# Kernel tuning notes

Hardware: AMD Instinct MI355X
Metric: run time of the kernel (lower is better)

## Reference

```python
import jax, jax.numpy as jnp
import numpy as np

B, N, K = 16, 4096, 32

def setup_inputs() -> dict:
    key = jax.random.key(0)
    k0, k1, k2, k3, k4, k5 = jax.random.split(key, 6)
    frames_rot = jax.random.normal(k0, (B, N, 3, 3), jnp.float32)
    frames_trans = jax.random.normal(k1, (B, N, 3), jnp.float32)
    pair_rot = jax.random.normal(k2, (B, N, K, 3, 3), jnp.float32)
    pair_trans = jax.random.normal(k3, (B, N, K, 3), jnp.float32)
    confidences = jax.random.uniform(k4, (B, N, K, 1), jnp.float32)
    topology = jax.random.randint(k5, (B, N, K), 0, N, jnp.int32)
    return {"frames_rot": frames_rot, "frames_trans": frames_trans,
            "pair_rot": pair_rot, "pair_trans": pair_trans,
            "confidences": confidences, "topology": topology}


def _proj_with_svd(m):
    """Kabsch projection of batched [..., 3, 3] matrices onto SO(3) (det=+1)."""
    u, s, vh = jnp.linalg.svd(m, full_matrices=False)
    V = jnp.swapaxes(vh, -1, -2)
    d = jnp.sign(jnp.linalg.det(jnp.matmul(V, jnp.swapaxes(u, -1, -2))))  # [...]
    d3 = jnp.concatenate([jnp.ones(d.shape + (2,), m.dtype), d[..., None]], axis=-1)  # diag(1,1,d)
    # rot = V @ diag(1,1,d) @ u^T
    return jnp.einsum('...ik,...k,...jk->...ij', V, d3, u)


def reference(frames_rot, frames_trans, pair_rot, pair_trans, confidences, topology):
    # gather neighbor frames T_j: [B,N,K,3,3] / [B,N,K,3]
    gather = jax.vmap(lambda f, t: f[t])
    Tj_rot = gather(frames_rot, topology)
    Tj_trans = gather(frames_trans, topology)

    # normalized confidences p_ij over neighbors K
    w = jnp.squeeze(confidences, axis=-1)             # [B,N,K]
    p = w / jnp.sum(w, axis=2, keepdims=True)         # [B,N,K]

    # compose rigids: T_j * T_ji
    comp_rot = jnp.einsum('bnkij,bnkjl->bnkil', Tj_rot, pair_rot)                 # [B,N,K,3,3]
    comp_trans = jnp.einsum('bnkij,bnkj->bnki', Tj_rot, pair_trans) + Tj_trans    # [B,N,K,3]

    # confidence-weighted average over neighbors
    avg_rot = jnp.einsum('bnk,bnkij->bnij', p, comp_rot)    # [B,N,3,3]
    avg_trans = jnp.einsum('bnk,bnki->bni', p, comp_trans)  # [B,N,3]

    # project averaged rot onto SO(3), then invert (transpose) as in the module
    rot = _proj_with_svd(avg_rot)
    rot_inv = jnp.swapaxes(rot, -1, -2)                     # invert_rots of a rotation

    # pack (rot 9 + trans 3) -> [B,N,12]
    return jnp.concatenate([rot_inv.reshape(B, N, 9), avg_trans], axis=-1)
```

## Files before the change

### kernel.cpp

```cpp
#include <hip/hip_runtime.h>
#include <math.h>

#define N_RES 4096
#define KNB 32
#define BN_TOTAL 65536

typedef float v4f __attribute__((ext_vector_type(4)));
typedef int v4i __attribute__((ext_vector_type(4)));

template <int p, int q>
__device__ __forceinline__ void jacobi_rot(float S[3][3], float V[3][3]) {
    float apq = S[p][q];
    if (fabsf(apq) > 1e-20f) {
        float app = S[p][p], aqq = S[q][q];
        float tau = (aqq - app) / (2.0f * apq);
        float tt = (tau >= 0.0f ? 1.0f : -1.0f) / (fabsf(tau) + sqrtf(1.0f + tau * tau));
        float c = 1.0f / sqrtf(1.0f + tt * tt);
        float s = tt * c;
#pragma unroll
        for (int i = 0; i < 3; i++) {
            float Sip = S[i][p], Siq = S[i][q];
            S[i][p] = c * Sip - s * Siq;
            S[i][q] = s * Sip + c * Siq;
        }
#pragma unroll
        for (int i = 0; i < 3; i++) {
            float Spi = S[p][i], Sqi = S[q][i];
            S[p][i] = c * Spi - s * Sqi;
            S[q][i] = s * Spi + c * Sqi;
        }
#pragma unroll
        for (int i = 0; i < 3; i++) {
            float Vip = V[i][p], Viq = V[i][q];
            V[i][p] = c * Vip - s * Viq;
            V[i][q] = s * Vip + c * Viq;
        }
    }
}

template <int A, int Bc>
__device__ __forceinline__ void sort_pair(float lam[3], float V[3][3]) {
    if (lam[A] < lam[Bc]) {
        float tl = lam[A]; lam[A] = lam[Bc]; lam[Bc] = tl;
#pragma unroll
        for (int i = 0; i < 3; i++) {
            float tv = V[i][A]; V[i][A] = V[i][Bc]; V[i][Bc] = tv;
        }
    }
}

__global__ __launch_bounds__(256) void backbone_kernel(
    const float* __restrict__ frames_rot,
    const float* __restrict__ frames_trans,
    const float* __restrict__ pair_rot,
    const float* __restrict__ pair_trans,
    const float* __restrict__ conf,
    const int* __restrict__ topo,
    float* __restrict__ out)
{
    int tid = threadIdx.x;
    int bid = blockIdx.x;

    int xcd = bid & 7;
    int slot = bid >> 3;
    int batch = xcd + ((slot >> 7) << 3);
    int chunk = slot & 127;

    int elem = batch * N_RES + chunk * 32 + (tid >> 3);
    int t = tid & 7;

    const float* fr_b = frames_rot + (size_t)batch * N_RES * 9;
    const float* ft_b = frames_trans + (size_t)batch * N_RES * 3;

    size_t kbase = (size_t)elem * KNB + (size_t)t * 4;
    const v4f* pr4 = (const v4f*)(pair_rot + kbase * 9);
    const v4f* pt4 = (const v4f*)(pair_trans + kbase * 3);
    const v4f* cf4 = (const v4f*)(conf + kbase);
    const v4i* tp4 = (const v4i*)(topo + kbase);

    float prl[36];
#pragma unroll
    for (int i = 0; i < 9; i++) {
        v4f v = __builtin_nontemporal_load(pr4 + i);
        prl[4 * i + 0] = v.x; prl[4 * i + 1] = v.y;
        prl[4 * i + 2] = v.z; prl[4 * i + 3] = v.w;
    }
    float ptl[12];
#pragma unroll
    for (int i = 0; i < 3; i++) {
        v4f v = __builtin_nontemporal_load(pt4 + i);
        ptl[4 * i + 0] = v.x; ptl[4 * i + 1] = v.y;
        ptl[4 * i + 2] = v.z; ptl[4 * i + 3] = v.w;
    }
    v4f wv = __builtin_nontemporal_load(cf4);
    float wl[4] = {wv.x, wv.y, wv.z, wv.w};
    v4i jv = __builtin_nontemporal_load(tp4);
    int jl[4] = {jv.x, jv.y, jv.z, jv.w};

    float Macc[9] = {0, 0, 0, 0, 0, 0, 0, 0, 0};
    float tacc[3] = {0, 0, 0};
    float wsum = 0.0f;

#pragma unroll
    for (int kk = 0; kk < 4; kk++) {
        int j = jl[kk];
        const float* Rj = fr_b + j * 9;
        const float* Tj = ft_b + j * 3;
        float r[9];
#pragma unroll
        for (int i = 0; i < 9; i++) r[i] = Rj[i];
        float tj[3];
#pragma unroll
        for (int i = 0; i < 3; i++) tj[i] = Tj[i];
        float w = wl[kk];
        const float* pr = prl + kk * 9;
        const float* pt = ptl + kk * 3;
#pragma unroll
        for (int i = 0; i < 3; i++) {
#pragma unroll
            for (int l = 0; l < 3; l++) {
                float cij = r[i * 3 + 0] * pr[0 * 3 + l] +
                            r[i * 3 + 1] * pr[1 * 3 + l] +
                            r[i * 3 + 2] * pr[2 * 3 + l];
                Macc[i * 3 + l] += w * cij;
            }
            float ct = r[i * 3 + 0] * pt[0] + r[i * 3 + 1] * pt[1] +
                       r[i * 3 + 2] * pt[2] + tj[i];
            tacc[i] += w * ct;
        }
        wsum += w;
    }

#pragma unroll
    for (int st = 1; st <= 4; st <<= 1) {
#pragma unroll
        for (int i = 0; i < 9; i++) Macc[i] += __shfl_xor(Macc[i], st);
#pragma unroll
        for (int i = 0; i < 3; i++) tacc[i] += __shfl_xor(tacc[i], st);
        wsum += __shfl_xor(wsum, st);
    }

    float inv_w = 1.0f / fmaxf(wsum, 1e-20f);
    float M[3][3];
#pragma unroll
    for (int i = 0; i < 3; i++)
#pragma unroll
        for (int j = 0; j < 3; j++) M[i][j] = Macc[i * 3 + j] * inv_w;
    float t0 = tacc[0] * inv_w, t1 = tacc[1] * inv_w, t2 = tacc[2] * inv_w;

    float S[3][3];
#pragma unroll
    for (int i = 0; i < 3; i++)
#pragma unroll
        for (int j = 0; j < 3; j++)
            S[i][j] = M[0][i] * M[0][j] + M[1][i] * M[1][j] + M[2][i] * M[2][j];
    float V[3][3] = {{1, 0, 0}, {0, 1, 0}, {0, 0, 1}};

#pragma unroll
    for (int sweep = 0; sweep < 4; sweep++) {
        jacobi_rot<0, 1>(S, V);
        jacobi_rot<0, 2>(S, V);
        jacobi_rot<1, 2>(S, V);
    }

    float lam[3] = {S[0][0], S[1][1], S[2][2]};
    sort_pair<0, 1>(lam, V);
    sort_pair<1, 2>(lam, V);
    sort_pair<0, 1>(lam, V);

    float detV = V[0][0] * (V[1][1] * V[2][2] - V[1][2] * V[2][1]) -
                 V[0][1] * (V[1][0] * V[2][2] - V[1][2] * V[2][0]) +
                 V[0][2] * (V[1][0] * V[2][1] - V[1][1] * V[2][0]);
    if (detV < 0.0f) { V[0][2] = -V[0][2]; V[1][2] = -V[1][2]; V[2][2] = -V[2][2]; }

    float Bm[3][3];
#pragma unroll
    for (int i = 0; i < 3; i++)
#pragma unroll
        for (int j = 0; j < 3; j++)
            Bm[i][j] = M[i][0] * V[0][j] + M[i][1] * V[1][j] + M[i][2] * V[2][j];

    float u0[3] = {Bm[0][0], Bm[1][0], Bm[2][0]};
    float n0 = u0[0] * u0[0] + u0[1] * u0[1] + u0[2] * u0[2];
    float rn0 = 1.0f / sqrtf(fmaxf(n0, 1e-24f));
    u0[0] *= rn0; u0[1] *= rn0; u0[2] *= rn0;

    float b1[3] = {Bm[0][1], Bm[1][1], Bm[2][1]};
    float d01 = u0[0] * b1[0] + u0[1] * b1[1] + u0[2] * b1[2];
    float u1[3] = {b1[0] - d01 * u0[0], b1[1] - d01 * u0[1], b1[2] - d01 * u0[2]};
    float n1 = u1[0] * u1[0] + u1[1] * u1[1] + u1[2] * u1[2];
    float rn1 = 1.0f / sqrtf(fmaxf(n1, 1e-24f));
    u1[0] *= rn1; u1[1] *= rn1; u1[2] *= rn1;

    float u2[3] = {u0[1] * u1[2] - u0[2] * u1[1],
                   u0[2] * u1[0] - u0[0] * u1[2],
                   u0[0] * u1[1] - u0[1] * u1[0]};

    float R[9];
#pragma unroll
    for (int i = 0; i < 3; i++) {
        float Ui0 = (i == 0 ? u0[0] : (i == 1 ? u0[1] : u0[2]));
        float Ui1 = (i == 0 ? u1[0] : (i == 1 ? u1[1] : u1[2]));
        float Ui2 = (i == 0 ? u2[0] : (i == 1 ? u2[1] : u2[2]));
#pragma unroll
        for (int j = 0; j < 3; j++)
            R[i * 3 + j] = Ui0 * V[j][0] + Ui1 * V[j][1] + Ui2 * V[j][2];
    }

    if (t == 0) {
        float4* o4 = (float4*)(out + (size_t)elem * 12);
        o4[0] = make_float4(R[0], R[1], R[2], R[3]);
        o4[1] = make_float4(R[4], R[5], R[6], R[7]);
        o4[2] = make_float4(R[8], t0, t1, t2);
    }
}

extern "C" void kernel_launch(void* const* d_in, const int* in_sizes, int n_in,
                              void* d_out, int out_size, void* d_ws, size_t ws_size,
                              hipStream_t stream) {
    const float* frames_rot = (const float*)d_in[0];
    const float* frames_trans = (const float*)d_in[1];
    const float* pair_rot = (const float*)d_in[2];
    const float* pair_trans = (const float*)d_in[3];
    const float* conf = (const float*)d_in[4];
    const int* topo = (const int*)d_in[5];
    float* out = (float*)d_out;

    dim3 grid(BN_TOTAL * 8 / 256), block(256);
    hipLaunchKernelGGL(backbone_kernel, grid, block, 0, stream,
                       frames_rot, frames_trans, pair_rot, pair_trans, conf, topo, out);
}
```

Before: 198.2 us.

## Split into repack, accumulate, and solve kernels with padded frame layout

Adds a repack kernel that copies frame rotation and translation into 16-float aligned rows so neighbour gathers become three 16-byte vector loads. Accumulation becomes its own kernel that writes per-element sums to workspace, and a separate solve kernel runs the Jacobi SVD projection with one thread per element, so seven of every eight lanes no longer sit idle through it. This costs two extra launches and extra workspace traffic for the repacked frames and accumulators. The original fused kernel is kept as a fallback when workspace is too small.

```diff
diff --git a/kernel.cpp b/kernel.cpp
--- a/kernel.cpp
+++ b/kernel.cpp
@@ -49,14 +49,96 @@
     }
 }
 
-__global__ __launch_bounds__(256) void backbone_kernel(
+__device__ __forceinline__ void project_and_store(const float M[3][3],
+                                                  float t0, float t1, float t2,
+                                                  float* outp) {
+    float S[3][3];
+#pragma unroll
+    for (int i = 0; i < 3; i++)
+#pragma unroll
+        for (int j = 0; j < 3; j++)
+            S[i][j] = M[0][i] * M[0][j] + M[1][i] * M[1][j] + M[2][i] * M[2][j];
+    float V[3][3] = {{1, 0, 0}, {0, 1, 0}, {0, 0, 1}};
+
+#pragma unroll
+    for (int sweep = 0; sweep < 4; sweep++) {
+        jacobi_rot<0, 1>(S, V);
+        jacobi_rot<0, 2>(S, V);
+        jacobi_rot<1, 2>(S, V);
+    }
+
+    float lam[3] = {S[0][0], S[1][1], S[2][2]};
+    sort_pair<0, 1>(lam, V);
+    sort_pair<1, 2>(lam, V);
+    sort_pair<0, 1>(lam, V);
+
+    float detV = V[0][0] * (V[1][1] * V[2][2] - V[1][2] * V[2][1]) -
+                 V[0][1] * (V[1][0] * V[2][2] - V[1][2] * V[2][0]) +
+                 V[0][2] * (V[1][0] * V[2][1] - V[1][1] * V[2][0]);
+    if (detV < 0.0f) { V[0][2] = -V[0][2]; V[1][2] = -V[1][2]; V[2][2] = -V[2][2]; }
+
+    float Bm[3][3];
+#pragma unroll
+    for (int i = 0; i < 3; i++)
+#pragma unroll
+        for (int j = 0; j < 3; j++)
+            Bm[i][j] = M[i][0] * V[0][j] + M[i][1] * V[1][j] + M[i][2] * V[2][j];
+
+    float u0[3] = {Bm[0][0], Bm[1][0], Bm[2][0]};
+    float n0 = u0[0] * u0[0] + u0[1] * u0[1] + u0[2] * u0[2];
+    float rn0 = 1.0f / sqrtf(fmaxf(n0, 1e-24f));
+    u0[0] *= rn0; u0[1] *= rn0; u0[2] *= rn0;
+
+    float b1[3] = {Bm[0][1], Bm[1][1], Bm[2][1]};
+    float d01 = u0[0] * b1[0] + u0[1] * b1[1] + u0[2] * b1[2];
+    float u1[3] = {b1[0] - d01 * u0[0], b1[1] - d01 * u0[1], b1[2] - d01 * u0[2]};
+    float n1 = u1[0] * u1[0] + u1[1] * u1[1] + u1[2] * u1[2];
+    float rn1 = 1.0f / sqrtf(fmaxf(n1, 1e-24f));
+    u1[0] *= rn1; u1[1] *= rn1; u1[2] *= rn1;
+
+    float u2[3] = {u0[1] * u1[2] - u0[2] * u1[1],
+                   u0[2] * u1[0] - u0[0] * u1[2],
+                   u0[0] * u1[1] - u0[1] * u1[0]};
+
+    float R[9];
+#pragma unroll
+    for (int i = 0; i < 3; i++) {
+        float Ui0 = (i == 0 ? u0[0] : (i == 1 ? u0[1] : u0[2]));
+        float Ui1 = (i == 0 ? u1[0] : (i == 1 ? u1[1] : u1[2]));
+        float Ui2 = (i == 0 ? u2[0] : (i == 1 ? u2[1] : u2[2]));
+#pragma unroll
+        for (int j = 0; j < 3; j++)
+            R[i * 3 + j] = Ui0 * V[j][0] + Ui1 * V[j][1] + Ui2 * V[j][2];
+    }
+
+    v4f* o4 = (v4f*)outp;
+    o4[0] = (v4f){R[0], R[1], R[2], R[3]};
+    o4[1] = (v4f){R[4], R[5], R[6], R[7]};
+    o4[2] = (v4f){R[8], t0, t1, t2};
+}
+
+__global__ __launch_bounds__(256) void repack_kernel(
     const float* __restrict__ frames_rot,
     const float* __restrict__ frames_trans,
+    float* __restrict__ pk)
+{
+    int row = blockIdx.x * 256 + threadIdx.x;
+    const float* fr = frames_rot + (size_t)row * 9;
+    const float* ft = frames_trans + (size_t)row * 3;
+    v4f a = {fr[0], fr[1], fr[2], fr[3]};
+    v4f b = {fr[4], fr[5], fr[6], fr[7]};
+    v4f c = {fr[8], ft[0], ft[1], ft[2]};
+    v4f* o = (v4f*)(pk + (size_t)row * 16);
+    o[0] = a; o[1] = b; o[2] = c;
+}
+
+__global__ __launch_bounds__(256) void accum_kernel(
+    const float* __restrict__ pk,
     const float* __restrict__ pair_rot,
     const float* __restrict__ pair_trans,
     const float* __restrict__ conf,
     const int* __restrict__ topo,
-    float* __restrict__ out)
+    float* __restrict__ acc)
 {
     int tid = threadIdx.x;
     int bid = blockIdx.x;
@@ -68,9 +150,6 @@
 
     int elem = batch * N_RES + chunk * 32 + (tid >> 3);
     int t = tid & 7;
-
-    const float* fr_b = frames_rot + (size_t)batch * N_RES * 9;
-    const float* ft_b = frames_trans + (size_t)batch * N_RES * 3;
 
     size_t kbase = (size_t)elem * KNB + (size_t)t * 4;
     const v4f* pr4 = (const v4f*)(pair_rot + kbase * 9);
@@ -101,17 +180,16 @@
     float tacc[3] = {0, 0, 0};
     float wsum = 0.0f;
 
+    size_t pkbase = (size_t)batch * N_RES * 16;
+
 #pragma unroll
     for (int kk = 0; kk < 4; kk++) {
         int j = jl[kk];
-        const float* Rj = fr_b + j * 9;
-        const float* Tj = ft_b + j * 3;
-        float r[9];
-#pragma unroll
-        for (int i = 0; i < 9; i++) r[i] = Rj[i];
-        float tj[3];
-#pragma unroll
-        for (int i = 0; i < 3; i++) tj[i] = Tj[i];
+        const v4f* row = (const v4f*)(pk + pkbase + (size_t)j * 16);
+        v4f fa = row[0], fb = row[1], fc = row[2];
+        float r[9] = {fa.x, fa.y, fa.z, fa.w, fb.x, fb.y, fb.z, fb.w, fc.x};
+        float tj[3] = {fc.y, fc.z, fc.w};
+
         float w = wl[kk];
         const float* pr = prl + kk * 9;
         const float* pt = ptl + kk * 3;
@@ -140,79 +218,121 @@
         wsum += __shfl_xor(wsum, st);
     }
 
+    if (t == 0) {
+        v4f* o = (v4f*)(acc + (size_t)elem * 16);
+        o[0] = (v4f){Macc[0], Macc[1], Macc[2], Macc[3]};
+        o[1] = (v4f){Macc[4], Macc[5], Macc[6], Macc[7]};
+        o[2] = (v4f){Macc[8], tacc[0], tacc[1], tacc[2]};
+        o[3] = (v4f){wsum, 0.0f, 0.0f, 0.0f};
+    }
+}
+
+__global__ __launch_bounds__(256) void solve_kernel(
+    const float* __restrict__ acc,
+    float* __restrict__ out)
+{
+    int elem = blockIdx.x * 256 + threadIdx.x;
+    const v4f* a4 = (const v4f*)(acc + (size_t)elem * 16);
+    v4f A0 = a4[0], A1 = a4[1], A2 = a4[2], A3 = a4[3];
+    float inv_w = 1.0f / fmaxf(A3.x, 1e-20f);
+    float M[3][3] = {{A0.x * inv_w, A0.y * inv_w, A0.z * inv_w},
+                     {A0.w * inv_w, A1.x * inv_w, A1.y * inv_w},
+                     {A1.z * inv_w, A1.w * inv_w, A2.x * inv_w}};
+    float t0 = A2.y * inv_w, t1 = A2.z * inv_w, t2 = A2.w * inv_w;
+    project_and_store(M, t0, t1, t2, out + (size_t)elem * 12);
+}
+
+__global__ __launch_bounds__(256) void fused_kernel(
+    const float* __restrict__ frames_rot, const float* __restrict__ frames_trans,
+    const float* __restrict__ pair_rot, const float* __restrict__ pair_trans,
+    const float* __restrict__ conf, const int* __restrict__ topo,
+    float* __restrict__ out)
+{
+    int tid = threadIdx.x;
+    int bid = blockIdx.x;
+    int xcd = bid & 7;
+    int slot = bid >> 3;
+    int batch = xcd + ((slot >> 7) << 3);
+    int chunk = slot & 127;
+    int elem = batch * N_RES + chunk * 32 + (tid >> 3);
+    int t = tid & 7;
+
+    const float* fr_b = frames_rot + (size_t)batch * N_RES * 9;
+    const float* ft_b = frames_trans + (size_t)batch * N_RES * 3;
+
+    size_t kbase = (size_t)elem * KNB + (size_t)t * 4;
+    const v4f* pr4 = (const v4f*)(pair_rot + kbase * 9);
+    const v4f* pt4 = (const v4f*)(pair_trans + kbase * 3);
+    const v4f* cf4 = (const v4f*)(conf + kbase);
+    const v4i* tp4 = (const v4i*)(topo + kbase);
+
+    float prl[36];
+#pragma unroll
+    for (int i = 0; i < 9; i++) {
+        v4f v = __builtin_nontemporal_load(pr4 + i);
+        prl[4 * i] = v.x; prl[4 * i + 1] = v.y; prl[4 * i + 2] = v.z; prl[4 * i + 3] = v.w;
+    }
+    float ptl[12];
+#pragma unroll
+    for (int i = 0; i < 3; i++) {
+        v4f v = __builtin_nontemporal_load(pt4 + i);
+        ptl[4 * i] = v.x; ptl[4 * i + 1] = v.y; ptl[4 * i + 2] = v.z; ptl[4 * i + 3] = v.w;
+    }
+    v4f wv = __builtin_nontemporal_load(cf4);
+    float wl[4] = {wv.x, wv.y, wv.z, wv.w};
+    v4i jv = __builtin_nontemporal_load(tp4);
+    int jl[4] = {jv.x, jv.y, jv.z, jv.w};
+
+    float Macc[9] = {0, 0, 0, 0, 0, 0, 0, 0, 0};
+    float tacc[3] = {0, 0, 0};
+    float wsum = 0.0f;
+
+#pragma unroll
+    for (int kk = 0; kk < 4; kk++) {
+        int j = jl[kk];
+        const float* Rj = fr_b + j * 9;
+        const float* Tj = ft_b + j * 3;
+        float r[9];
+#pragma unroll
+        for (int i = 0; i < 9; i++) r[i] = Rj[i];
+        float tj[3];
+#pragma unroll
+        for (int i = 0; i < 3; i++) tj[i] = Tj[i];
+        float w = wl[kk];
+        const float* pr = prl + kk * 9;
+        const float* pt = ptl + kk * 3;
+#pragma unroll
+        for (int i = 0; i < 3; i++) {
+#pragma unroll
+            for (int l = 0; l < 3; l++) {
+                float cij = r[i * 3] * pr[l] + r[i * 3 + 1] * pr[3 + l] + r[i * 3 + 2] * pr[6 + l];
+                Macc[i * 3 + l] += w * cij;
+            }
+            float ct = r[i * 3] * pt[0] + r[i * 3 + 1] * pt[1] + r[i * 3 + 2] * pt[2] + tj[i];
+            tacc[i] += w * ct;
+        }
+        wsum += w;
+    }
+
+#pragma unroll
+    for (int st = 1; st <= 4; st <<= 1) {
+#pragma unroll
+        for (int i = 0; i < 9; i++) Macc[i] += __shfl_xor(Macc[i], st);
+#pragma unroll
+        for (int i = 0; i < 3; i++) tacc[i] += __shfl_xor(tacc[i], st);
+        wsum += __shfl_xor(wsum, st);
+    }
+
     float inv_w = 1.0f / fmaxf(wsum, 1e-20f);
     float M[3][3];
 #pragma unroll
     for (int i = 0; i < 3; i++)
 #pragma unroll
         for (int j = 0; j < 3; j++) M[i][j] = Macc[i * 3 + j] * inv_w;
-    float t0 = tacc[0] * inv_w, t1 = tacc[1] * inv_w, t2 = tacc[2] * inv_w;
-
-    float S[3][3];
-#pragma unroll
-    for (int i = 0; i < 3; i++)
-#pragma unroll
-        for (int j = 0; j < 3; j++)
-            S[i][j] = M[0][i] * M[0][j] + M[1][i] * M[1][j] + M[2][i] * M[2][j];
-    float V[3][3] = {{1, 0, 0}, {0, 1, 0}, {0, 0, 1}};
-
-#pragma unroll
-    for (int sweep = 0; sweep < 4; sweep++) {
-        jacobi_rot<0, 1>(S, V);
-        jacobi_rot<0, 2>(S, V);
-        jacobi_rot<1, 2>(S, V);
-    }
-
-    float lam[3] = {S[0][0], S[1][1], S[2][2]};
-    sort_pair<0, 1>(lam, V);
-    sort_pair<1, 2>(lam, V);
-    sort_pair<0, 1>(lam, V);
-
-    float detV = V[0][0] * (V[1][1] * V[2][2] - V[1][2] * V[2][1]) -
-                 V[0][1] * (V[1][0] * V[2][2] - V[1][2] * V[2][0]) +
-                 V[0][2] * (V[1][0] * V[2][1] - V[1][1] * V[2][0]);
-    if (detV < 0.0f) { V[0][2] = -V[0][2]; V[1][2] = -V[1][2]; V[2][2] = -V[2][2]; }
-
-    float Bm[3][3];
-#pragma unroll
-    for (int i = 0; i < 3; i++)
-#pragma unroll
-        for (int j = 0; j < 3; j++)
-            Bm[i][j] = M[i][0] * V[0][j] + M[i][1] * V[1][j] + M[i][2] * V[2][j];
-
-    float u0[3] = {Bm[0][0], Bm[1][0], Bm[2][0]};
-    float n0 = u0[0] * u0[0] + u0[1] * u0[1] + u0[2] * u0[2];
-    float rn0 = 1.0f / sqrtf(fmaxf(n0, 1e-24f));
-    u0[0] *= rn0; u0[1] *= rn0; u0[2] *= rn0;
-
-    float b1[3] = {Bm[0][1], Bm[1][1], Bm[2][1]};
-    float d01 = u0[0] * b1[0] + u0[1] * b1[1] + u0[2] * b1[2];
-    float u1[3] = {b1[0] - d01 * u0[0], b1[1] - d01 * u0[1], b1[2] - d01 * u0[2]};
-    float n1 = u1[0] * u1[0] + u1[1] * u1[1] + u1[2] * u1[2];
-    float rn1 = 1.0f / sqrtf(fmaxf(n1, 1e-24f));
-    u1[0] *= rn1; u1[1] *= rn1; u1[2] *= rn1;
-
-    float u2[3] = {u0[1] * u1[2] - u0[2] * u1[1],
-                   u0[2] * u1[0] - u0[0] * u1[2],
-                   u0[0] * u1[1] - u0[1] * u1[0]};
-
-    float R[9];
-#pragma unroll
-    for (int i = 0; i < 3; i++) {
-        float Ui0 = (i == 0 ? u0[0] : (i == 1 ? u0[1] : u0[2]));
-        float Ui1 = (i == 0 ? u1[0] : (i == 1 ? u1[1] : u1[2]));
-        float Ui2 = (i == 0 ? u2[0] : (i == 1 ? u2[1] : u2[2]));
-#pragma unroll
-        for (int j = 0; j < 3; j++)
-            R[i * 3 + j] = Ui0 * V[j][0] + Ui1 * V[j][1] + Ui2 * V[j][2];
-    }
-
-    if (t == 0) {
-        float4* o4 = (float4*)(out + (size_t)elem * 12);
-        o4[0] = make_float4(R[0], R[1], R[2], R[3]);
-        o4[1] = make_float4(R[4], R[5], R[6], R[7]);
-        o4[2] = make_float4(R[8], t0, t1, t2);
-    }
+
+    if (t == 0)
+        project_and_store(M, tacc[0] * inv_w, tacc[1] * inv_w, tacc[2] * inv_w,
+                          out + (size_t)elem * 12);
 }
 
 extern "C" void kernel_launch(void* const* d_in, const int* in_sizes, int n_in,
@@ -226,7 +346,20 @@
     const int* topo = (const int*)d_in[5];
     float* out = (float*)d_out;
 
-    dim3 grid(BN_TOTAL * 8 / 256), block(256);
-    hipLaunchKernelGGL(backbone_kernel, grid, block, 0, stream,
-                       frames_rot, frames_trans, pair_rot, pair_trans, conf, topo, out);
-}
+    const size_t PK_BYTES = (size_t)BN_TOTAL * 16 * sizeof(float);
+    const size_t need = 2 * PK_BYTES;
+
+    if (ws_size >= need) {
+        float* pk = (float*)d_ws;
+        float* acc = pk + (size_t)BN_TOTAL * 16;
+        hipLaunchKernelGGL(repack_kernel, dim3(BN_TOTAL / 256), dim3(256), 0, stream,
+                           frames_rot, frames_trans, pk);
+        hipLaunchKernelGGL(accum_kernel, dim3(BN_TOTAL * 8 / 256), dim3(256), 0, stream,
+                           pk, pair_rot, pair_trans, conf, topo, acc);
+        hipLaunchKernelGGL(solve_kernel, dim3(BN_TOTAL / 256), dim3(256), 0, stream,
+                           acc, out);
+    } else {
+        hipLaunchKernelGGL(fused_kernel, dim3(BN_TOTAL * 8 / 256), dim3(256), 0, stream,
+                           frames_rot, frames_trans, pair_rot, pair_trans, conf, topo, out);
+    }
+}
```

Result: slower. 202.5 us (+2.2%).
